# Performance work log

Measured on AMD Instinct MI355X. Metric: run time of the kernel, lower is better.

The kernel has to match this reference:

```python
import jax, jax.numpy as jnp
import numpy as np

N_NODES = 50000
N_EDGES = 1600000
IN_CH, OUT_CH, SIZE = 128, 64, 4


def _segment_softmax(e, seg, n):
    # numerically stable softmax of edge scores grouped by segment id (PyG softmax)
    m = jax.ops.segment_max(e, seg, num_segments=n)
    ex = jnp.exp(e - m[seg])
    s = jax.ops.segment_sum(ex, seg, num_segments=n)
    return ex / (s[seg] + 1e-16)


def setup_inputs() -> dict:
    key = jax.random.key(0)
    k = jax.random.split(key, 6)
    x = jax.random.normal(k[0], (N_NODES, IN_CH), dtype=jnp.float32)
    edge_index = jax.random.randint(k[1], (2, N_EDGES), 0, N_NODES, dtype=jnp.int64)
    W = jax.random.normal(k[2], (SIZE, IN_CH, OUT_CH), dtype=jnp.float32) * 0.1
    att_src = jax.random.normal(k[3], (SIZE, OUT_CH), dtype=jnp.float32) * 0.1
    att_dst = jax.random.normal(k[4], (SIZE, OUT_CH), dtype=jnp.float32) * 0.1
    bias = jnp.zeros((SIZE, OUT_CH), dtype=jnp.float32)
    return {"x": x, "W": W, "att_src": att_src, "att_dst": att_dst,
            "bias": bias, "edge_index": edge_index, "direction": 1}


def reference(x, W, att_src, att_dst, bias, edge_index, direction):
    src, dst = edge_index[0], edge_index[1]
    n = x.shape[0]
    size = W.shape[0]
    feat_sum = None
    att_sum = None
    for i in range(size):  # small fixed ensemble of GATConv layers
        h = x @ W[i]                                    # [N, out]
        a_s = h @ att_src[i]                            # [N] source scores
        a_d = h @ att_dst[i]                            # [N] target scores
        e = jax.nn.leaky_relu(a_s[src] + a_d[dst], 0.2)  # [E] GAT slope 0.2
        alpha = _segment_softmax(e, dst, n)             # softmax over incoming edges
        out = jax.ops.segment_sum(alpha[:, None] * h[src], dst, num_segments=n) + bias[i]
        fl = jax.nn.leaky_relu(out, 0.01)               # f.leaky_relu default slope
        feat_sum = fl if feat_sum is None else feat_sum + fl
        att_sum = alpha if att_sum is None else att_sum + alpha
    # directional node pooling: mean of summed edge attention grouped by source node
    counts = jax.ops.segment_sum(jnp.ones_like(att_sum), src, num_segments=n)
    pooled = jax.ops.segment_sum(att_sum, src, num_segments=n) / jnp.maximum(counts, 1.0)
    node_scores = direction * pooled
    return feat_sum, node_scores
```

## Files before the change

kernel.cpp:

```cpp
#include <hip/hip_runtime.h>
#include <stdint.h>

#define N_NODES 50000
#define N_EDGES 1600000
#define IN_CH   128
#define OUT_CH  64
#define CAP     72
#define NBUCKET 196
#define BCAP    10240
#define MB      782
#define EPB2    2047
#define BKCAP   32
#define NODES_PAD (NBUCKET * 256)
#define SENTINEL 0xFFFFFFFFu

typedef float  f32x4  __attribute__((ext_vector_type(4)));
typedef __bf16 bf16x8 __attribute__((ext_vector_type(8)));
typedef unsigned short u16x8 __attribute__((ext_vector_type(8)));

__device__ __forceinline__ unsigned int f2bf(float f) {
    unsigned int u = __float_as_uint(f);
    u += 0x7fffu + ((u >> 16) & 1u);
    return u >> 16;
}
__device__ __forceinline__ float lrelu(float v, float s) { return v > 0.f ? v : s * v; }

__device__ __forceinline__ void split2(float f, unsigned short& hi, unsigned short& lo) {
    unsigned int u = __float_as_uint(f);
    hi = (unsigned short)(u >> 16);
    float r = f - __uint_as_float(u & 0xffff0000u);
    lo = (unsigned short)f2bf(r);
}

#define POOL_SCALE 268435456.0f
#define POOL_MASK  ((1ull << 40) - 1ull)

__global__ __launch_bounds__(256, 1) void k_gemmbin(
    const float* __restrict__ x, const float* __restrict__ W,
    const float* __restrict__ att_src, const float* __restrict__ att_dst,
    unsigned short* __restrict__ H, float* __restrict__ a_s, float* __restrict__ a_d,
    const int* __restrict__ ei, int* __restrict__ gcur,
    unsigned int* __restrict__ binned)
{
    __shared__ __align__(16) unsigned char smem[64 * 264 * 2];
    float* sx = (float*)smem;

    const int tid  = threadIdx.x;
    const int lane = tid & 63;
    const int lr   = lane & 15;
    const int lg   = lane >> 4;
    const int wv   = __builtin_amdgcn_readfirstlane(tid >> 6);
    const int row0 = blockIdx.x * 64;

    for (int idx = tid; idx < 64 * 32; idx += 256) {
        int r = idx >> 5, c4 = idx & 31;
        int row = row0 + r;
        float4 v = make_float4(0.f, 0.f, 0.f, 0.f);
        if (row < N_NODES) v = ((const float4*)(x + (size_t)row * IN_CH))[c4];
        *(float4*)(sx + r * 132 + c4 * 4) = v;
    }
    __syncthreads();

    f32x4 acc[4][4];
#pragma unroll
    for (int m = 0; m < 4; ++m)
#pragma unroll
        for (int n = 0; n < 4; ++n) acc[m][n] = (f32x4){0.f, 0.f, 0.f, 0.f};

    const float* Wl = W + (size_t)wv * IN_CH * OUT_CH;

#pragma unroll 1
    for (int ks = 0; ks < 4; ++ks) {
        bf16x8 ahi[4], alo[4];
#pragma unroll
        for (int m = 0; m < 4; ++m) {
            const float* xr = sx + (m * 16 + lr) * 132 + ks * 32 + lg * 8;
            float4 xa = *(const float4*)xr;
            float4 xb = *(const float4*)(xr + 4);
            float xs[8] = {xa.x, xa.y, xa.z, xa.w, xb.x, xb.y, xb.z, xb.w};
            u16x8 h, l;
#pragma unroll
            for (int j = 0; j < 8; ++j) {
                unsigned short a, b; split2(xs[j], a, b); h[j] = a; l[j] = b;
            }
            ahi[m] = __builtin_bit_cast(bf16x8, h);
            alo[m] = __builtin_bit_cast(bf16x8, l);
        }
#pragma unroll
        for (int n = 0; n < 4; ++n) {
            const float* wb = Wl + (size_t)(ks * 32 + lg * 8) * OUT_CH + n * 16 + lr;
            u16x8 h, l;
#pragma unroll
            for (int j = 0; j < 8; ++j) {
                unsigned short a, b; split2(wb[j * OUT_CH], a, b); h[j] = a; l[j] = b;
            }
            bf16x8 bhi = __builtin_bit_cast(bf16x8, h);
            bf16x8 blo = __builtin_bit_cast(bf16x8, l);
#pragma unroll
            for (int m = 0; m < 4; ++m) {
                acc[m][n] = __builtin_amdgcn_mfma_f32_16x16x32_bf16(ahi[m], bhi, acc[m][n], 0, 0, 0);
                acc[m][n] = __builtin_amdgcn_mfma_f32_16x16x32_bf16(alo[m], bhi, acc[m][n], 0, 0, 0);
                acc[m][n] = __builtin_amdgcn_mfma_f32_16x16x32_bf16(ahi[m], blo, acc[m][n], 0, 0, 0);
            }
        }
    }

    float As_c[4], Ad_c[4];
#pragma unroll
    for (int n = 0; n < 4; ++n) {
        As_c[n] = att_src[wv * OUT_CH + n * 16 + lr];
        Ad_c[n] = att_dst[wv * OUT_CH + n * 16 + lr];
    }
    float ps[16], pd[16];
#pragma unroll
    for (int m = 0; m < 4; ++m)
#pragma unroll
        for (int q = 0; q < 4; ++q) {
            float s = 0.f, d = 0.f;
#pragma unroll
            for (int n = 0; n < 4; ++n) {
                s = fmaf(acc[m][n][q], As_c[n], s);
                d = fmaf(acc[m][n][q], Ad_c[n], d);
            }
            ps[m * 4 + q] = s; pd[m * 4 + q] = d;
        }
#pragma unroll
    for (int off = 1; off <= 8; off <<= 1) {
#pragma unroll
        for (int i = 0; i < 16; ++i) {
            ps[i] += __shfl_xor(ps[i], off);
            pd[i] += __shfl_xor(pd[i], off);
        }
    }
    float vs = ps[0], vd = pd[0];
#pragma unroll
    for (int i = 1; i < 16; ++i) {
        bool e = (lr == i);
        vs = e ? ps[i] : vs;
        vd = e ? pd[i] : vd;
    }
    {
        int rg = row0 + (lr >> 2) * 16 + lg * 4 + (lr & 3);
        if (rg < N_NODES) { a_s[rg * 4 + wv] = vs; a_d[rg * 4 + wv] = vd; }
    }

    __syncthreads();
    unsigned short* shs = (unsigned short*)smem;
#pragma unroll
    for (int m = 0; m < 4; ++m)
#pragma unroll
        for (int n = 0; n < 4; ++n)
#pragma unroll
            for (int q = 0; q < 4; ++q)
                shs[(m * 16 + lg * 4 + q) * 264 + wv * 64 + n * 16 + lr] =
                    (unsigned short)f2bf(acc[m][n][q]);
    __syncthreads();

    for (int idx = tid; idx < 64 * 32; idx += 256) {
        int r = idx >> 5, c8 = idx & 31;
        int row2 = row0 + r;
        if (row2 < N_NODES) {
            const uint4* srcp = (const uint4*)(shs + r * 264);
            ((uint4*)(H + (size_t)row2 * 256))[c8] = srcp[c8];
        }
    }
    __syncthreads();

    int* lcnt = (int*)smem;
    unsigned int* stage = (unsigned int*)(smem + 1024);
    const int start = blockIdx.x * EPB2;
    const int end = (start + EPB2 < N_EDGES) ? start + EPB2 : N_EDGES;

    int probe = ei[2 * (start + tid) + 1];
    const int is64 = (__ballot(probe != 0) == 0ull) ? 1 : 0;

    for (int i = tid; i < NBUCKET; i += 256) lcnt[i] = 0;
    __syncthreads();

    for (int e = start + tid; e < end; e += 256) {
        int s = is64 ? ei[2 * (long long)e] : ei[e];
        int d = is64 ? ei[2 * ((long long)N_EDGES + e)] : ei[N_EDGES + e];
        int bk = d >> 8;
        unsigned int pk = ((unsigned int)s << 16) | (unsigned int)d;
        int pos = atomicAdd(&lcnt[bk], 1);
        if (pos < BKCAP) {
            stage[pos * 256 + bk] = pk;
        } else {
            int gi = atomicAdd(&gcur[bk], 4);
            if (gi + 3 < BCAP) {
                unsigned int* q = binned + bk * BCAP + gi;
                q[0] = pk; q[1] = SENTINEL; q[2] = SENTINEL; q[3] = SENTINEL;
            }
        }
    }
    __syncthreads();

    if (tid < NBUCKET) {
        int c = lcnt[tid];
        if (c > BKCAP) c = BKCAP;
        int cpad = (c + 3) & ~3;
        if (cpad) {
            int base = atomicAdd(&gcur[tid], cpad);
            if (base + cpad <= BCAP) {
                uint4* dst = (uint4*)(binned + tid * BCAP + base);
                for (int p = 0; p < c; p += 4) {
                    uint4 v;
                    v.x = stage[p * 256 + tid];
                    v.y = (p + 1 < c) ? stage[(p + 1) * 256 + tid] : SENTINEL;
                    v.z = (p + 2 < c) ? stage[(p + 2) * 256 + tid] : SENTINEL;
                    v.w = (p + 3 < c) ? stage[(p + 3) * 256 + tid] : SENTINEL;
                    dst[p >> 2] = v;
                }
            }
        }
    }
}

__global__ __launch_bounds__(256) void k_bucket(
    const unsigned int* __restrict__ binned, const int* __restrict__ gcur,
    unsigned short* __restrict__ slot, int* __restrict__ cnt_dst,
    unsigned long long* __restrict__ pool)
{
    __shared__ unsigned short sl[256 * CAP];
    __shared__ int cnt[256];
    const int b = blockIdx.x;
    const int tid = threadIdx.x;
    cnt[tid] = 0;
    int pidx = b * 256 + tid;
    if (pidx < N_NODES) pool[pidx] = 0ull;
    __syncthreads();

    int total = gcur[b];
    if (total > BCAP) total = BCAP;
    const unsigned int* src = binned + b * BCAP;
    for (int i = tid; i < total; i += 256) {
        unsigned int p = src[i];
        if (p == SENTINEL) continue;
        int local = p & 255;
        int pos = atomicAdd(&cnt[local], 1);
        if (pos < CAP) sl[local * CAP + pos] = (unsigned short)(p >> 16);
    }
    __syncthreads();

    uint4* g = (uint4*)(slot + (size_t)b * 256 * CAP);
    const uint4* l = (const uint4*)sl;
    for (int i = tid; i < 256 * CAP * 2 / 16; i += 256) g[i] = l[i];
    cnt_dst[b * 256 + tid] = cnt[tid];
}

__global__ __launch_bounds__(256) void k_gather(
    const unsigned short* __restrict__ H, const unsigned short* __restrict__ slot,
    const int* __restrict__ cnt_dst,
    const float* __restrict__ a_s, const float* __restrict__ a_d,
    const float* __restrict__ bias, unsigned long long* __restrict__ pool,
    float* __restrict__ out)
{
    __shared__ __align__(16) float ewlds[4][CAP * 4];

    const int lane = threadIdx.x & 63;
    const int wv = __builtin_amdgcn_readfirstlane(threadIdx.x >> 6);
    const int node = blockIdx.x * 4 + wv;
    int deg = __builtin_amdgcn_readfirstlane(cnt_dst[node]);
    if (deg > CAP) deg = CAP;
    const int layer = lane >> 4;
    float* ewl = ewlds[wv];

    const float4* as4p = (const float4*)a_s;
    const unsigned short* s16 = slot + (size_t)node * CAP;
    const float4 ad4 = ((const float4*)a_d)[node];

#pragma unroll
    for (int base = 0; base < CAP; base += 64) {
        int j = base + lane;
        if (j < deg) {
            int s = s16[j];
            float4 as4 = as4p[s];
            float t0 = as4.x + ad4.x, t1 = as4.y + ad4.y;
            float t2 = as4.z + ad4.z, t3 = as4.w + ad4.w;
            float4 e4;
            e4.x = __expf(fmaxf(t0, 0.2f * t0));
            e4.y = __expf(fmaxf(t1, 0.2f * t1));
            e4.z = __expf(fmaxf(t2, 0.2f * t2));
            e4.w = __expf(fmaxf(t3, 0.2f * t3));
            *(float4*)(ewl + j * 4) = e4;
        }
    }

    float ax = 0.f, ay = 0.f, az = 0.f, aw = 0.f, sumExp = 0.f;
    const uint2* Hp = (const uint2*)H + lane;

    auto body = [&](unsigned int s, int j) {
        float ew = ewl[j * 4 + layer];
        uint2 hv = Hp[(size_t)s * 64];
        ax = fmaf(ew, __uint_as_float(hv.x << 16), ax);
        ay = fmaf(ew, __uint_as_float(hv.x & 0xffff0000u), ay);
        az = fmaf(ew, __uint_as_float(hv.y << 16), az);
        aw = fmaf(ew, __uint_as_float(hv.y & 0xffff0000u), aw);
        sumExp += ew;
    };

    const unsigned int* sp = (const unsigned int*)s16;
    const int npair = deg >> 1;
    int j2 = 0;
    for (; j2 + 8 <= npair; j2 += 8) {
        uint4 pa = *(const uint4*)(sp + j2);
        uint4 pb = *(const uint4*)(sp + j2 + 4);
        body(pa.x & 0xffffu, 2*j2+0); body(pa.x >> 16, 2*j2+1);
        body(pa.y & 0xffffu, 2*j2+2); body(pa.y >> 16, 2*j2+3);
        body(pa.z & 0xffffu, 2*j2+4); body(pa.z >> 16, 2*j2+5);
        body(pa.w & 0xffffu, 2*j2+6); body(pa.w >> 16, 2*j2+7);
        body(pb.x & 0xffffu, 2*j2+8); body(pb.x >> 16, 2*j2+9);
        body(pb.y & 0xffffu, 2*j2+10); body(pb.y >> 16, 2*j2+11);
        body(pb.z & 0xffffu, 2*j2+12); body(pb.z >> 16, 2*j2+13);
        body(pb.w & 0xffffu, 2*j2+14); body(pb.w >> 16, 2*j2+15);
    }
    for (; j2 + 4 <= npair; j2 += 4) {
        uint4 p4 = *(const uint4*)(sp + j2);
        body(p4.x & 0xffffu, 2*j2+0); body(p4.x >> 16, 2*j2+1);
        body(p4.y & 0xffffu, 2*j2+2); body(p4.y >> 16, 2*j2+3);
        body(p4.z & 0xffffu, 2*j2+4); body(p4.z >> 16, 2*j2+5);
        body(p4.w & 0xffffu, 2*j2+6); body(p4.w >> 16, 2*j2+7);
    }
    for (; j2 < npair; ++j2) {
        unsigned int pr = sp[j2];
        body(pr & 0xffffu, 2*j2); body(pr >> 16, 2*j2+1);
    }
    if (deg & 1) body(sp[npair] & 0xffffu, deg - 1);

    float inv = 1.0f / (sumExp + 1e-16f);
    float4 b = ((const float4*)bias)[lane];
    float v0 = lrelu(fmaf(ax, inv, b.x), 0.01f);
    float v1 = lrelu(fmaf(ay, inv, b.y), 0.01f);
    float v2 = lrelu(fmaf(az, inv, b.z), 0.01f);
    float v3 = lrelu(fmaf(aw, inv, b.w), 0.01f);
    v0 += __shfl_xor(v0, 16); v0 += __shfl_xor(v0, 32);
    v1 += __shfl_xor(v1, 16); v1 += __shfl_xor(v1, 32);
    v2 += __shfl_xor(v2, 16); v2 += __shfl_xor(v2, 32);
    v3 += __shfl_xor(v3, 16); v3 += __shfl_xor(v3, 32);

    if (lane < 16) {
        ((float4*)(out + (size_t)node * 64))[lane] = make_float4(v0, v1, v2, v3);
    }

    float i0 = 1.0f / (__shfl(sumExp,  0) + 1e-16f);
    float i1 = 1.0f / (__shfl(sumExp, 16) + 1e-16f);
    float i2 = 1.0f / (__shfl(sumExp, 32) + 1e-16f);
    float i3 = 1.0f / (__shfl(sumExp, 48) + 1e-16f);
    for (int jj = lane; jj < deg; jj += 64) {
        int s = s16[jj];
        float4 e4 = *(const float4*)(ewl + jj * 4);
        float tot = e4.x * i0 + e4.y * i1 + e4.z * i2 + e4.w * i3;
        unsigned long long enc = (1ull << 40) |
            (unsigned long long)(tot * POOL_SCALE + 0.5f);
        atomicAdd(pool + s, enc);
    }
}

__global__ __launch_bounds__(256) void k_final(
    const unsigned long long* __restrict__ pool, const int* __restrict__ dirp,
    float* __restrict__ out)
{
    int i = blockIdx.x * 256 + threadIdx.x;
    if (i >= N_NODES) return;
    unsigned long long v = pool[i];
    unsigned int cnt = (unsigned int)(v >> 40);
    float val = (float)((double)(v & POOL_MASK) * (1.0 / (double)POOL_SCALE));
    int di = dirp[0];
    float dirf = (di >= -1000 && di <= 1000) ? (float)di : __int_as_float(di);
    float denom = (cnt > 1u) ? (float)cnt : 1.0f;
    out[(size_t)N_NODES * 64 + i] = dirf * val / denom;
}

extern "C" void kernel_launch(void* const* d_in, const int* in_sizes, int n_in,
                              void* d_out, int out_size, void* d_ws, size_t ws_size,
                              hipStream_t stream)
{
    const float* x       = (const float*)d_in[0];
    const float* W       = (const float*)d_in[1];
    const float* att_src = (const float*)d_in[2];
    const float* att_dst = (const float*)d_in[3];
    const float* bias    = (const float*)d_in[4];
    const int*   ei      = (const int*)d_in[5];
    const int*   dirp    = (const int*)d_in[6];
    float* out = (float*)d_out;

    char* w = (char*)d_ws;
    size_t off = 0;
    auto alloc = [&](size_t bytes) -> void* {
        void* p = w + off;
        off = (off + bytes + 255) & ~(size_t)255;
        return p;
    };
    int* gcur = (int*)alloc((size_t)NBUCKET * sizeof(int));
    unsigned long long* pool = (unsigned long long*)alloc((size_t)N_NODES * sizeof(unsigned long long));
    float* a_s = (float*)alloc((size_t)N_NODES * 4 * sizeof(float));
    float* a_d = (float*)alloc((size_t)N_NODES * 4 * sizeof(float));
    int* cnt_dst = (int*)alloc((size_t)NODES_PAD * sizeof(int));
    unsigned int* binned = (unsigned int*)alloc((size_t)NBUCKET * BCAP * sizeof(unsigned int));
    unsigned short* slot = (unsigned short*)alloc((size_t)NODES_PAD * CAP * sizeof(unsigned short));
    unsigned short* H = (unsigned short*)alloc((size_t)N_NODES * 256 * sizeof(unsigned short));
    (void)ws_size; (void)in_sizes; (void)n_in; (void)out_size;

    hipMemsetAsync(gcur, 0, NBUCKET * sizeof(int), stream);
    k_gemmbin<<<MB, 256, 0, stream>>>(x, W, att_src, att_dst, H, a_s, a_d, ei, gcur, binned);
    k_bucket<<<NBUCKET, 256, 0, stream>>>(binned, gcur, slot, cnt_dst, pool);
    k_gather<<<N_NODES / 4, 256, 0, stream>>>(H, slot, cnt_dst, a_s, a_d, bias, pool, out);
    k_final<<<(N_NODES + 255) / 256, 256, 0, stream>>>(pool, dirp, out);
}
```

Baseline: 266.4 us.

## Aggregate raw bf16 node features before the projection GEMM

This uses the linearity of the projection to change the order of work. Each destination node first gathers a softmax-weighted sum of the 128-channel bf16 inputs for each of the 4 layers, and only then multiplies by W with MFMA in a new output kernel that also adds bias, applies leaky-relu and does the pooling finalisation. The attention scores are computed from the precomputed products W·att_src and W·att_dst, and the edge binning moves into its own kernel. The aim is to halve the per-edge gather traffic from 512 B to 256 B rows and to drop the 3-pass split-precision GEMM on x. In exchange it writes and reads an extra 51 MB bf16 aggregate buffer and rounds both x and the aggregates to bf16, which costs accuracy.

```diff
diff --git a/kernel.cpp b/kernel.cpp
--- a/kernel.cpp
+++ b/kernel.cpp
@@ -9,6 +9,7 @@
 #define NBUCKET 196
 #define BCAP    10240
 #define MB      782
+#define NODES48 (MB * 64)
 #define EPB2    2047
 #define BKCAP   32
 #define NODES_PAD (NBUCKET * 256)
@@ -16,7 +17,6 @@
 
 typedef float  f32x4  __attribute__((ext_vector_type(4)));
 typedef __bf16 bf16x8 __attribute__((ext_vector_type(8)));
-typedef unsigned short u16x8 __attribute__((ext_vector_type(8)));
 
 __device__ __forceinline__ unsigned int f2bf(float f) {
     unsigned int u = __float_as_uint(f);
@@ -35,139 +35,80 @@
 #define POOL_SCALE 268435456.0f
 #define POOL_MASK  ((1ull << 40) - 1ull)
 
-__global__ __launch_bounds__(256, 1) void k_gemmbin(
-    const float* __restrict__ x, const float* __restrict__ W,
-    const float* __restrict__ att_src, const float* __restrict__ att_dst,
-    unsigned short* __restrict__ H, float* __restrict__ a_s, float* __restrict__ a_d,
-    const int* __restrict__ ei, int* __restrict__ gcur,
-    unsigned int* __restrict__ binned)
-{
-    __shared__ __align__(16) unsigned char smem[64 * 264 * 2];
-    float* sx = (float*)smem;
-
-    const int tid  = threadIdx.x;
-    const int lane = tid & 63;
-    const int lr   = lane & 15;
-    const int lg   = lane >> 4;
-    const int wv   = __builtin_amdgcn_readfirstlane(tid >> 6);
-    const int row0 = blockIdx.x * 64;
-
-    for (int idx = tid; idx < 64 * 32; idx += 256) {
-        int r = idx >> 5, c4 = idx & 31;
-        int row = row0 + r;
-        float4 v = make_float4(0.f, 0.f, 0.f, 0.f);
-        if (row < N_NODES) v = ((const float4*)(x + (size_t)row * IN_CH))[c4];
-        *(float4*)(sx + r * 132 + c4 * 4) = v;
-    }
-    __syncthreads();
-
-    f32x4 acc[4][4];
-#pragma unroll
-    for (int m = 0; m < 4; ++m)
-#pragma unroll
-        for (int n = 0; n < 4; ++n) acc[m][n] = (f32x4){0.f, 0.f, 0.f, 0.f};
-
-    const float* Wl = W + (size_t)wv * IN_CH * OUT_CH;
-
-#pragma unroll 1
-    for (int ks = 0; ks < 4; ++ks) {
-        bf16x8 ahi[4], alo[4];
-#pragma unroll
-        for (int m = 0; m < 4; ++m) {
-            const float* xr = sx + (m * 16 + lr) * 132 + ks * 32 + lg * 8;
-            float4 xa = *(const float4*)xr;
-            float4 xb = *(const float4*)(xr + 4);
-            float xs[8] = {xa.x, xa.y, xa.z, xa.w, xb.x, xb.y, xb.z, xb.w};
-            u16x8 h, l;
-#pragma unroll
-            for (int j = 0; j < 8; ++j) {
-                unsigned short a, b; split2(xs[j], a, b); h[j] = a; l[j] = b;
-            }
-            ahi[m] = __builtin_bit_cast(bf16x8, h);
-            alo[m] = __builtin_bit_cast(bf16x8, l);
-        }
-#pragma unroll
-        for (int n = 0; n < 4; ++n) {
-            const float* wb = Wl + (size_t)(ks * 32 + lg * 8) * OUT_CH + n * 16 + lr;
-            u16x8 h, l;
-#pragma unroll
-            for (int j = 0; j < 8; ++j) {
-                unsigned short a, b; split2(wb[j * OUT_CH], a, b); h[j] = a; l[j] = b;
-            }
-            bf16x8 bhi = __builtin_bit_cast(bf16x8, h);
-            bf16x8 blo = __builtin_bit_cast(bf16x8, l);
-#pragma unroll
-            for (int m = 0; m < 4; ++m) {
-                acc[m][n] = __builtin_amdgcn_mfma_f32_16x16x32_bf16(ahi[m], bhi, acc[m][n], 0, 0, 0);
-                acc[m][n] = __builtin_amdgcn_mfma_f32_16x16x32_bf16(alo[m], bhi, acc[m][n], 0, 0, 0);
-                acc[m][n] = __builtin_amdgcn_mfma_f32_16x16x32_bf16(ahi[m], blo, acc[m][n], 0, 0, 0);
-            }
-        }
-    }
-
-    float As_c[4], Ad_c[4];
-#pragma unroll
-    for (int n = 0; n < 4; ++n) {
-        As_c[n] = att_src[wv * OUT_CH + n * 16 + lr];
-        Ad_c[n] = att_dst[wv * OUT_CH + n * 16 + lr];
-    }
-    float ps[16], pd[16];
-#pragma unroll
-    for (int m = 0; m < 4; ++m)
-#pragma unroll
-        for (int q = 0; q < 4; ++q) {
-            float s = 0.f, d = 0.f;
-#pragma unroll
-            for (int n = 0; n < 4; ++n) {
-                s = fmaf(acc[m][n][q], As_c[n], s);
-                d = fmaf(acc[m][n][q], Ad_c[n], d);
-            }
-            ps[m * 4 + q] = s; pd[m * 4 + q] = d;
-        }
-#pragma unroll
-    for (int off = 1; off <= 8; off <<= 1) {
-#pragma unroll
-        for (int i = 0; i < 16; ++i) {
-            ps[i] += __shfl_xor(ps[i], off);
-            pd[i] += __shfl_xor(pd[i], off);
-        }
-    }
-    float vs = ps[0], vd = pd[0];
-#pragma unroll
-    for (int i = 1; i < 16; ++i) {
-        bool e = (lr == i);
-        vs = e ? ps[i] : vs;
-        vd = e ? pd[i] : vd;
-    }
+__global__ __launch_bounds__(256) void k_prep0(
+    const float* __restrict__ W, const float* __restrict__ att_src,
+    const float* __restrict__ att_dst,
+    unsigned short* __restrict__ Wh, unsigned short* __restrict__ Wl,
+    float* __restrict__ w_s, float* __restrict__ w_d, int* __restrict__ gcur)
+{
+    const int l = blockIdx.x;
+    const int tid = threadIdx.x;
+    const float* Wb = W + (size_t)l * IN_CH * OUT_CH;
+
+    for (int idx = tid; idx < IN_CH * OUT_CH; idx += 256) {
+        int c = idx >> 7, k = idx & 127;
+        unsigned short h, lo2;
+        split2(Wb[k * OUT_CH + c], h, lo2);
+        Wh[l * 8192 + idx] = h;
+        Wl[l * 8192 + idx] = lo2;
+    }
+    if (tid < IN_CH) {
+        float s = 0.f, d = 0.f;
+        const float* As = att_src + l * OUT_CH;
+        const float* Ad = att_dst + l * OUT_CH;
+        const float* wr = Wb + tid * OUT_CH;
+#pragma unroll 8
+        for (int c = 0; c < OUT_CH; ++c) { s = fmaf(wr[c], As[c], s); d = fmaf(wr[c], Ad[c], d); }
+        w_s[l * IN_CH + tid] = s;
+        w_d[l * IN_CH + tid] = d;
+    }
+    if (l == 0 && tid < NBUCKET) gcur[tid] = 0;
+}
+
+__global__ __launch_bounds__(256) void k_prepx(
+    const float* __restrict__ x, const float* __restrict__ w_s,
+    const float* __restrict__ w_d,
+    unsigned int* __restrict__ X16, float* __restrict__ a_s, float* __restrict__ a_d)
+{
+    const int lane = threadIdx.x & 63;
+    const int wv = __builtin_amdgcn_readfirstlane(threadIdx.x >> 6);
+    const int node = blockIdx.x * 4 + wv;
+    float2 xv = ((const float2*)(x + (size_t)node * IN_CH))[lane];
+    X16[(size_t)node * 64 + lane] = f2bf(xv.x) | (f2bf(xv.y) << 16);
+
+    float s0, s1, s2, s3, d0, d1, d2, d3;
     {
-        int rg = row0 + (lr >> 2) * 16 + lg * 4 + (lr & 3);
-        if (rg < N_NODES) { a_s[rg * 4 + wv] = vs; a_d[rg * 4 + wv] = vd; }
-    }
-
-    __syncthreads();
-    unsigned short* shs = (unsigned short*)smem;
-#pragma unroll
-    for (int m = 0; m < 4; ++m)
-#pragma unroll
-        for (int n = 0; n < 4; ++n)
-#pragma unroll
-            for (int q = 0; q < 4; ++q)
-                shs[(m * 16 + lg * 4 + q) * 264 + wv * 64 + n * 16 + lr] =
-                    (unsigned short)f2bf(acc[m][n][q]);
-    __syncthreads();
-
-    for (int idx = tid; idx < 64 * 32; idx += 256) {
-        int r = idx >> 5, c8 = idx & 31;
-        int row2 = row0 + r;
-        if (row2 < N_NODES) {
-            const uint4* srcp = (const uint4*)(shs + r * 264);
-            ((uint4*)(H + (size_t)row2 * 256))[c8] = srcp[c8];
-        }
-    }
-    __syncthreads();
-
-    int* lcnt = (int*)smem;
-    unsigned int* stage = (unsigned int*)(smem + 1024);
+        const float2* ws = (const float2*)w_s + lane;
+        const float2* wd = (const float2*)w_d + lane;
+        float2 a;
+        a = ws[0];   s0 = xv.x * a.x + xv.y * a.y;
+        a = ws[64];  s1 = xv.x * a.x + xv.y * a.y;
+        a = ws[128]; s2 = xv.x * a.x + xv.y * a.y;
+        a = ws[192]; s3 = xv.x * a.x + xv.y * a.y;
+        a = wd[0];   d0 = xv.x * a.x + xv.y * a.y;
+        a = wd[64];  d1 = xv.x * a.x + xv.y * a.y;
+        a = wd[128]; d2 = xv.x * a.x + xv.y * a.y;
+        a = wd[192]; d3 = xv.x * a.x + xv.y * a.y;
+    }
+#pragma unroll
+    for (int off = 1; off <= 32; off <<= 1) {
+        s0 += __shfl_xor(s0, off); s1 += __shfl_xor(s1, off);
+        s2 += __shfl_xor(s2, off); s3 += __shfl_xor(s3, off);
+        d0 += __shfl_xor(d0, off); d1 += __shfl_xor(d1, off);
+        d2 += __shfl_xor(d2, off); d3 += __shfl_xor(d3, off);
+    }
+    if (lane == 0) {
+        float* ap = a_s + node * 4; ap[0] = s0; ap[1] = s1; ap[2] = s2; ap[3] = s3;
+        float* dp = a_d + node * 4; dp[0] = d0; dp[1] = d1; dp[2] = d2; dp[3] = d3;
+    }
+}
+
+__global__ __launch_bounds__(256) void k_bin(
+    const int* __restrict__ ei, int* __restrict__ gcur, unsigned int* __restrict__ binned)
+{
+    __shared__ int lcnt[NBUCKET];
+    __shared__ unsigned int stage[BKCAP * 256];
+    const int tid = threadIdx.x;
     const int start = blockIdx.x * EPB2;
     const int end = (start + EPB2 < N_EDGES) ? start + EPB2 : N_EDGES;
 
@@ -249,11 +190,10 @@
 }
 
 __global__ __launch_bounds__(256) void k_gather(
-    const unsigned short* __restrict__ H, const unsigned short* __restrict__ slot,
+    const unsigned int* __restrict__ X16, const unsigned short* __restrict__ slot,
     const int* __restrict__ cnt_dst,
     const float* __restrict__ a_s, const float* __restrict__ a_d,
-    const float* __restrict__ bias, unsigned long long* __restrict__ pool,
-    float* __restrict__ out)
+    unsigned long long* __restrict__ pool, unsigned int* __restrict__ AG)
 {
     __shared__ __align__(16) float ewlds[4][CAP * 4];
 
@@ -262,13 +202,13 @@
     const int node = blockIdx.x * 4 + wv;
     int deg = __builtin_amdgcn_readfirstlane(cnt_dst[node]);
     if (deg > CAP) deg = CAP;
-    const int layer = lane >> 4;
     float* ewl = ewlds[wv];
 
     const float4* as4p = (const float4*)a_s;
     const unsigned short* s16 = slot + (size_t)node * CAP;
     const float4 ad4 = ((const float4*)a_d)[node];
 
+    float se0 = 0.f, se1 = 0.f, se2 = 0.f, se3 = 0.f;
 #pragma unroll
     for (int base = 0; base < CAP; base += 64) {
         int j = base + lane;
@@ -283,20 +223,32 @@
             e4.z = __expf(fmaxf(t2, 0.2f * t2));
             e4.w = __expf(fmaxf(t3, 0.2f * t3));
             *(float4*)(ewl + j * 4) = e4;
-        }
-    }
-
-    float ax = 0.f, ay = 0.f, az = 0.f, aw = 0.f, sumExp = 0.f;
-    const uint2* Hp = (const uint2*)H + lane;
+            se0 += e4.x; se1 += e4.y; se2 += e4.z; se3 += e4.w;
+        }
+    }
+#pragma unroll
+    for (int off = 1; off <= 32; off <<= 1) {
+        se0 += __shfl_xor(se0, off); se1 += __shfl_xor(se1, off);
+        se2 += __shfl_xor(se2, off); se3 += __shfl_xor(se3, off);
+    }
+    const float i0 = 1.0f / (se0 + 1e-16f);
+    const float i1 = 1.0f / (se1 + 1e-16f);
+    const float i2 = 1.0f / (se2 + 1e-16f);
+    const float i3 = 1.0f / (se3 + 1e-16f);
+
+    float a00 = 0.f, a01 = 0.f, a10 = 0.f, a11 = 0.f;
+    float a20 = 0.f, a21 = 0.f, a30 = 0.f, a31 = 0.f;
+    const unsigned int* Xp = X16 + lane;
 
     auto body = [&](unsigned int s, int j) {
-        float ew = ewl[j * 4 + layer];
-        uint2 hv = Hp[(size_t)s * 64];
-        ax = fmaf(ew, __uint_as_float(hv.x << 16), ax);
-        ay = fmaf(ew, __uint_as_float(hv.x & 0xffff0000u), ay);
-        az = fmaf(ew, __uint_as_float(hv.y << 16), az);
-        aw = fmaf(ew, __uint_as_float(hv.y & 0xffff0000u), aw);
-        sumExp += ew;
+        float4 e4 = *(const float4*)(ewl + j * 4);
+        unsigned int xv = Xp[(size_t)s * 64];
+        float x0 = __uint_as_float(xv << 16);
+        float x1 = __uint_as_float(xv & 0xffff0000u);
+        a00 = fmaf(e4.x, x0, a00); a01 = fmaf(e4.x, x1, a01);
+        a10 = fmaf(e4.y, x0, a10); a11 = fmaf(e4.y, x1, a11);
+        a20 = fmaf(e4.z, x0, a20); a21 = fmaf(e4.z, x1, a21);
+        a30 = fmaf(e4.w, x0, a30); a31 = fmaf(e4.w, x1, a31);
     };
 
     const unsigned int* sp = (const unsigned int*)s16;
@@ -327,25 +279,12 @@
     }
     if (deg & 1) body(sp[npair] & 0xffffu, deg - 1);
 
-    float inv = 1.0f / (sumExp + 1e-16f);
-    float4 b = ((const float4*)bias)[lane];
-    float v0 = lrelu(fmaf(ax, inv, b.x), 0.01f);
-    float v1 = lrelu(fmaf(ay, inv, b.y), 0.01f);
-    float v2 = lrelu(fmaf(az, inv, b.z), 0.01f);
-    float v3 = lrelu(fmaf(aw, inv, b.w), 0.01f);
-    v0 += __shfl_xor(v0, 16); v0 += __shfl_xor(v0, 32);
-    v1 += __shfl_xor(v1, 16); v1 += __shfl_xor(v1, 32);
-    v2 += __shfl_xor(v2, 16); v2 += __shfl_xor(v2, 32);
-    v3 += __shfl_xor(v3, 16); v3 += __shfl_xor(v3, 32);
-
-    if (lane < 16) {
-        ((float4*)(out + (size_t)node * 64))[lane] = make_float4(v0, v1, v2, v3);
-    }
-
-    float i0 = 1.0f / (__shfl(sumExp,  0) + 1e-16f);
-    float i1 = 1.0f / (__shfl(sumExp, 16) + 1e-16f);
-    float i2 = 1.0f / (__shfl(sumExp, 32) + 1e-16f);
-    float i3 = 1.0f / (__shfl(sumExp, 48) + 1e-16f);
+    unsigned int* agp = AG + ((size_t)node * 4) * 64 + lane;
+    agp[0]   = f2bf(a00 * i0) | (f2bf(a01 * i0) << 16);
+    agp[64]  = f2bf(a10 * i1) | (f2bf(a11 * i1) << 16);
+    agp[128] = f2bf(a20 * i2) | (f2bf(a21 * i2) << 16);
+    agp[192] = f2bf(a30 * i3) | (f2bf(a31 * i3) << 16);
+
     for (int jj = lane; jj < deg; jj += 64) {
         int s = s16[jj];
         float4 e4 = *(const float4*)(ewl + jj * 4);
@@ -356,19 +295,81 @@
     }
 }
 
-__global__ __launch_bounds__(256) void k_final(
+__global__ __launch_bounds__(256, 1) void k_out(
+    const unsigned short* __restrict__ AG, const unsigned short* __restrict__ Wh,
+    const unsigned short* __restrict__ Wl, const float* __restrict__ bias,
     const unsigned long long* __restrict__ pool, const int* __restrict__ dirp,
     float* __restrict__ out)
 {
-    int i = blockIdx.x * 256 + threadIdx.x;
-    if (i >= N_NODES) return;
-    unsigned long long v = pool[i];
-    unsigned int cnt = (unsigned int)(v >> 40);
-    float val = (float)((double)(v & POOL_MASK) * (1.0 / (double)POOL_SCALE));
-    int di = dirp[0];
-    float dirf = (di >= -1000 && di <= 1000) ? (float)di : __int_as_float(di);
-    float denom = (cnt > 1u) ? (float)cnt : 1.0f;
-    out[(size_t)N_NODES * 64 + i] = dirf * val / denom;
+    __shared__ float red[4][64][68];
+    const int tid = threadIdx.x;
+    const int lane = tid & 63;
+    const int lr = lane & 15, lg = lane >> 4;
+    const int wv = __builtin_amdgcn_readfirstlane(tid >> 6);
+    const int row0 = blockIdx.x * 64;
+
+    f32x4 acc[4][4];
+#pragma unroll
+    for (int m = 0; m < 4; ++m)
+#pragma unroll
+        for (int n = 0; n < 4; ++n) acc[m][n] = (f32x4){0.f, 0.f, 0.f, 0.f};
+
+    const unsigned short* Whl = Wh + wv * 8192;
+    const unsigned short* Wll = Wl + wv * 8192;
+#pragma unroll
+    for (int ks = 0; ks < 4; ++ks) {
+        bf16x8 afr[4];
+#pragma unroll
+        for (int m = 0; m < 4; ++m) {
+            size_t node = row0 + m * 16 + lr;
+            afr[m] = *(const bf16x8*)(AG + (node * 4 + wv) * 128 + ks * 32 + lg * 8);
+        }
+#pragma unroll
+        for (int n = 0; n < 4; ++n) {
+            int off = (n * 16 + lr) * 128 + ks * 32 + lg * 8;
+            bf16x8 bhi = *(const bf16x8*)(Whl + off);
+            bf16x8 blo = *(const bf16x8*)(Wll + off);
+#pragma unroll
+            for (int m = 0; m < 4; ++m) {
+                acc[m][n] = __builtin_amdgcn_mfma_f32_16x16x32_bf16(afr[m], bhi, acc[m][n], 0, 0, 0);
+                acc[m][n] = __builtin_amdgcn_mfma_f32_16x16x32_bf16(afr[m], blo, acc[m][n], 0, 0, 0);
+            }
+        }
+    }
+
+    float bn[4];
+#pragma unroll
+    for (int n = 0; n < 4; ++n) bn[n] = bias[wv * OUT_CH + n * 16 + lr];
+#pragma unroll
+    for (int m = 0; m < 4; ++m)
+#pragma unroll
+        for (int n = 0; n < 4; ++n)
+#pragma unroll
+            for (int q = 0; q < 4; ++q)
+                red[wv][m * 16 + lg * 4 + q][n * 16 + lr] =
+                    lrelu(acc[m][n][q] + bn[n], 0.01f);
+    __syncthreads();
+
+    for (int i = tid; i < 64 * 64; i += 256) {
+        int r = i >> 6, c = i & 63;
+        int node = row0 + r;
+        if (node < N_NODES)
+            out[(size_t)node * 64 + c] =
+                red[0][r][c] + red[1][r][c] + red[2][r][c] + red[3][r][c];
+    }
+
+    if (tid < 64) {
+        int node = row0 + tid;
+        if (node < N_NODES) {
+            unsigned long long v = pool[node];
+            unsigned int cnt = (unsigned int)(v >> 40);
+            float val = (float)((double)(v & POOL_MASK) * (1.0 / (double)POOL_SCALE));
+            int di = dirp[0];
+            float dirf = (di >= -1000 && di <= 1000) ? (float)di : __int_as_float(di);
+            float denom = (cnt > 1u) ? (float)cnt : 1.0f;
+            out[(size_t)N_NODES * 64 + node] = dirf * val / denom;
+        }
+    }
 }
 
 extern "C" void kernel_launch(void* const* d_in, const int* in_sizes, int n_in,
@@ -396,14 +397,21 @@
     float* a_s = (float*)alloc((size_t)N_NODES * 4 * sizeof(float));
     float* a_d = (float*)alloc((size_t)N_NODES * 4 * sizeof(float));
     int* cnt_dst = (int*)alloc((size_t)NODES_PAD * sizeof(int));
-    unsigned int* binned = (unsigned int*)alloc((size_t)NBUCKET * BCAP * sizeof(unsigned int));
     unsigned short* slot = (unsigned short*)alloc((size_t)NODES_PAD * CAP * sizeof(unsigned short));
-    unsigned short* H = (unsigned short*)alloc((size_t)N_NODES * 256 * sizeof(unsigned short));
+    unsigned int* X16 = (unsigned int*)alloc((size_t)NODES48 * 64 * sizeof(unsigned int));
+    unsigned short* Wh = (unsigned short*)alloc((size_t)4 * 8192 * sizeof(unsigned short));
+    unsigned short* Wl = (unsigned short*)alloc((size_t)4 * 8192 * sizeof(unsigned short));
+    float* w_s = (float*)alloc((size_t)4 * IN_CH * sizeof(float));
+    float* w_d = (float*)alloc((size_t)4 * IN_CH * sizeof(float));
+    unsigned short* AG = (unsigned short*)alloc((size_t)NODES48 * 4 * IN_CH * sizeof(unsigned short));
+    unsigned int* binned = (unsigned int*)AG;
     (void)ws_size; (void)in_sizes; (void)n_in; (void)out_size;
 
-    hipMemsetAsync(gcur, 0, NBUCKET * sizeof(int), stream);
-    k_gemmbin<<<MB, 256, 0, stream>>>(x, W, att_src, att_dst, H, a_s, a_d, ei, gcur, binned);
+    k_prep0<<<4, 256, 0, stream>>>(W, att_src, att_dst, Wh, Wl, w_s, w_d, gcur);
+    k_prepx<<<N_NODES / 4, 256, 0, stream>>>(x, w_s, w_d, X16, a_s, a_d);
+    k_bin<<<MB, 256, 0, stream>>>(ei, gcur, binned);
     k_bucket<<<NBUCKET, 256, 0, stream>>>(binned, gcur, slot, cnt_dst, pool);
-    k_gather<<<N_NODES / 4, 256, 0, stream>>>(H, slot, cnt_dst, a_s, a_d, bias, pool, out);
-    k_final<<<(N_NODES + 255) / 256, 256, 0, stream>>>(pool, dirp, out);
-}
+    k_gather<<<N_NODES / 4, 256, 0, stream>>>(X16, slot, cnt_dst, a_s, a_d, pool,
+                                              (unsigned int*)AG);
+    k_out<<<MB, 256, 0, stream>>>(AG, Wh, Wl, bias, pool, dirp, out);
+}
```

Result: no change. 268.9 us (+1.0%).
